# Kernel optimization log

Measured on AMD Instinct MI355X. Metric: run time of the kernel, lower is better.

## Reference

```python
import jax, jax.numpy as jnp
import numpy as np

FEAT_STRIDE = 16
PRE_NMS_TOP_N = 6000
POST_NMS_TOP_N = 300
NMS_THRESH = 0.7
MIN_SIZE = 16.0
SCALES = np.array([8.0, 16.0, 32.0])
RATIOS = np.array([0.5, 1.0, 2.0])


def _whctrs(a):
    w = a[2] - a[0] + 1.0
    h = a[3] - a[1] + 1.0
    return w, h, a[0] + 0.5 * (w - 1.0), a[1] + 0.5 * (h - 1.0)


def _mkanchors(ws, hs, xc, yc):
    ws = np.asarray(ws).reshape(-1, 1)
    hs = np.asarray(hs).reshape(-1, 1)
    return np.hstack([xc - 0.5 * (ws - 1.0), yc - 0.5 * (hs - 1.0),
                      xc + 0.5 * (ws - 1.0), yc + 0.5 * (hs - 1.0)])


def generate_anchors(base_size, ratios, scales):
    base = np.array([1.0, 1.0, base_size, base_size]) - 1.0
    w, h, xc, yc = _whctrs(base)
    size = w * h
    ws = np.round(np.sqrt(size / ratios))
    hs = np.round(ws * ratios)
    ratio_anchors = _mkanchors(ws, hs, xc, yc)
    out = []
    for i in range(ratio_anchors.shape[0]):
        w, h, xc, yc = _whctrs(ratio_anchors[i])
        out.append(_mkanchors(w * scales, h * scales, xc, yc))
    return np.vstack(out)


def _nms(boxes, scores, thresh, max_out):
    # greedy NMS, boxes [N,4], scores [N] (-inf = invalid). Returns idx [max_out], valid [max_out]
    N = boxes.shape[0]
    x1, y1, x2, y2 = boxes[:, 0], boxes[:, 1], boxes[:, 2], boxes[:, 3]
    areas = (x2 - x1 + 1.0) * (y2 - y1 + 1.0)
    ar = jnp.arange(N)

    def step(s, _):
        i = jnp.argmax(s)
        valid = s[i] > -jnp.inf
        b = boxes[i]
        xx1 = jnp.maximum(b[0], x1)
        yy1 = jnp.maximum(b[1], y1)
        xx2 = jnp.minimum(b[2], x2)
        yy2 = jnp.minimum(b[3], y2)
        inter = jnp.maximum(0.0, xx2 - xx1 + 1.0) * jnp.maximum(0.0, yy2 - yy1 + 1.0)
        iou = inter / (areas[i] + areas - inter)
        sup = (iou > thresh) | (ar == i)
        return jnp.where(sup, -jnp.inf, s), (i, valid)

    _, (idx, valid) = jax.lax.scan(step, scores, None, length=max_out)
    return idx, valid


def setup_inputs() -> dict:
    key = jax.random.key(0)
    k1, k2 = jax.random.split(key)
    B, A, Hf, Wf = 16, 9, 160, 160
    scores_map = jax.random.uniform(k1, (B, 2 * A, Hf, Wf), dtype=jnp.float32)
    bbox_deltas = jax.random.normal(k2, (B, 4 * A, Hf, Wf), dtype=jnp.float32) * 0.2
    im_info = jnp.tile(jnp.array([[Hf * FEAT_STRIDE, Wf * FEAT_STRIDE, 1.0]], jnp.float32), (B, 1))
    return {"scores_map": scores_map, "bbox_deltas": bbox_deltas, "im_info": im_info}


def reference(scores_map, bbox_deltas, im_info):
    anchors0 = jnp.asarray(generate_anchors(16, RATIOS, SCALES), jnp.float32)  # [A,4]
    A = anchors0.shape[0]
    B, _, Hf, Wf = scores_map.shape
    # fg scores: [B, A, H, W] -> [B, H*W*A]
    scores = scores_map[:, A:].transpose(0, 2, 3, 1).reshape(B, -1)
    deltas = bbox_deltas.transpose(0, 2, 3, 1).reshape(B, -1, 4)  # [B, H*W*A, 4]
    sx = (jnp.arange(Wf) * FEAT_STRIDE).astype(jnp.float32)
    sy = (jnp.arange(Hf) * FEAT_STRIDE).astype(jnp.float32)
    SX, SY = jnp.meshgrid(sx, sy)  # [H, W]
    shifts = jnp.stack([SX.ravel(), SY.ravel(), SX.ravel(), SY.ravel()], axis=1)  # [K,4]
    all_anchors = (shifts[:, None, :] + anchors0[None, :, :]).reshape(-1, 4)  # [K*A, 4]

    aw = all_anchors[:, 2] - all_anchors[:, 0] + 1.0
    ah = all_anchors[:, 3] - all_anchors[:, 1] + 1.0
    acx = all_anchors[:, 0] + 0.5 * aw
    acy = all_anchors[:, 1] + 0.5 * ah

    def single(s, d, info):
        # bbox_transform_inv
        pcx = d[:, 0] * aw + acx
        pcy = d[:, 1] * ah + acy
        pw = jnp.exp(d[:, 2]) * aw
        ph = jnp.exp(d[:, 3]) * ah
        x1 = jnp.clip(pcx - 0.5 * pw, 0.0, info[1] - 1.0)
        y1 = jnp.clip(pcy - 0.5 * ph, 0.0, info[0] - 1.0)
        x2 = jnp.clip(pcx + 0.5 * pw, 0.0, info[1] - 1.0)
        y2 = jnp.clip(pcy + 0.5 * ph, 0.0, info[0] - 1.0)
        boxes = jnp.stack([x1, y1, x2, y2], axis=1)
        ms = MIN_SIZE * info[2]
        keep = ((x2 - x1 + 1.0) >= ms) & ((y2 - y1 + 1.0) >= ms)
        s = jnp.where(keep, s, -jnp.inf)
        top_s, top_i = jax.lax.top_k(s, PRE_NMS_TOP_N)
        top_b = boxes[top_i]
        idx, valid = _nms(top_b, top_s, NMS_THRESH, POST_NMS_TOP_N)
        return jnp.where(valid[:, None], top_b[idx], 0.0)  # [POST, 4]

    out_boxes = jax.vmap(single)(scores, deltas, im_info)  # [B, POST, 4]
    batch_col = jnp.broadcast_to(
        jnp.arange(B, dtype=out_boxes.dtype)[:, None, None], (B, POST_NMS_TOP_N, 1))
    return jnp.concatenate([batch_col, out_boxes], axis=2)  # [B, POST, 5]
```

## Files before the change

### kernel.cpp

```cpp
#include <hip/hip_runtime.h>
#include <cstdint>
#include <cstddef>

typedef unsigned int u32;
typedef unsigned short u16;
typedef unsigned long long u64;

#define NBATCH 16
#define NA 9
#define HF 160
#define WF 160
#define HWC (HF*WF)
#define NPB (NA*HWC)
#define PRE_N 6000
#define POST_N 300
#define SEL_CAP 8192
#define NBIN 2048
#define UNI_BINS 1024
#define HSLICES 45
#define NMS_W 16
#define CHUNK 512


__constant__ float c_AW[9] = {184.f,368.f,736.f,128.f,256.f,512.f,88.f,176.f,352.f};
__constant__ float c_AH[9] = {96.f,192.f,384.f,128.f,256.f,512.f,176.f,352.f,704.f};

__device__ __forceinline__ void box_core(
    float d0, float d1, float d2, float d3, int a, int x, int y,
    float imH, float imW, float ms,
    float& x1, float& y1, float& x2, float& y2, bool& keep)
{
  float aw = c_AW[a], ah = c_AH[a];
  float acx = (float)x * 16.0f + 8.0f;
  float acy = (float)y * 16.0f + 8.0f;
  float pcx = d0 * aw + acx;
  float pcy = d1 * ah + acy;
  float pw  = expf(d2) * aw;
  float ph  = expf(d3) * ah;
  x1 = fminf(fmaxf(pcx - 0.5f * pw, 0.0f), imW - 1.0f);
  y1 = fminf(fmaxf(pcy - 0.5f * ph, 0.0f), imH - 1.0f);
  x2 = fminf(fmaxf(pcx + 0.5f * pw, 0.0f), imW - 1.0f);
  y2 = fminf(fmaxf(pcy + 0.5f * ph, 0.0f), imH - 1.0f);
  keep = ((x2 - x1 + 1.0f) >= ms) && ((y2 - y1 + 1.0f) >= ms);
}

__device__ __forceinline__ void box_from_deltas(
    const float* __restrict__ bd, int b, int a, int pos,
    float imH, float imW, float ms,
    float& x1, float& y1, float& x2, float& y2, bool& keep)
{
  int y = pos / WF;
  int x = pos - y * WF;
  size_t base = ((size_t)(b * 4 * NA) + 4 * a) * HWC + (size_t)pos;
  float d0 = bd[base];
  float d1 = bd[base + HWC];
  float d2 = bd[base + 2 * HWC];
  float d3 = bd[base + 3 * HWC];
  box_core(d0, d1, d2, d3, a, x, y, imH, imW, ms, x1, y1, x2, y2, keep);
}

__device__ __forceinline__ u32 desc_enc(float s) {
  u32 su = __float_as_uint(s);
  u32 asc = (su & 0x80000000u) ? ~su : (su | 0x80000000u);
  return ~asc;
}

__device__ __forceinline__ bool iou_gt(float inter, float uni) {
  float ss = fmaf(0.7f, uni, -inter);
  if (fabsf(ss) <= uni * 1e-6f) return (inter / uni > 0.7f);
  return ss < 0.0f;
}

__global__ void __launch_bounds__(256) k_scores_hist(
    const float* __restrict__ sm, const float* __restrict__ bd,
    const float* __restrict__ info, u32* __restrict__ keys, u32* __restrict__ hist) {
  __shared__ u32 lh[UNI_BINS];
  int img   = blockIdx.x / HSLICES;
  int rem   = blockIdx.x - img * HSLICES;
  int a     = rem / 5;
  int chunk = rem - a * 5;
  int tid = threadIdx.x;
  for (int i = tid; i < UNI_BINS; i += 256) lh[i] = 0;
  __syncthreads();
  float imH = info[img*3+0], imW = info[img*3+1], ms = 16.0f * info[img*3+2];
  const float* sp = sm + ((size_t)(img * 2 * NA) + NA + a) * HWC;
  const float* dp = bd + ((size_t)(img * 4 * NA) + 4 * a) * HWC;
  u32* kp = keys + (size_t)img * NPB + (size_t)a * HWC;
  for (int j = 0; j < 5; j++) {
    int pos0 = (chunk * 1280 + j * 256 + tid) * 4;
    float4 s4  = *(const float4*)&sp[pos0];
    float4 q0  = *(const float4*)&dp[pos0];
    float4 q1  = *(const float4*)&dp[HWC + pos0];
    float4 q2  = *(const float4*)&dp[2*HWC + pos0];
    float4 q3  = *(const float4*)&dp[3*HWC + pos0];
    float sv[4] = {s4.x, s4.y, s4.z, s4.w};
    float v0[4] = {q0.x, q0.y, q0.z, q0.w};
    float v1[4] = {q1.x, q1.y, q1.z, q1.w};
    float v2[4] = {q2.x, q2.y, q2.z, q2.w};
    float v3[4] = {q3.x, q3.y, q3.z, q3.w};
    u32 kq[4];
    #pragma unroll
    for (int e = 0; e < 4; e++) {
      int pos = pos0 + e;
      int y = pos / WF;
      int x = pos - y * WF;
      float x1, y1, x2, y2; bool keep;
      box_core(v0[e], v1[e], v2[e], v3[e], a, x, y, imH, imW, ms, x1, y1, x2, y2, keep);
      float s = sv[e];
      if (!keep) s = __uint_as_float(0xFF800000u);
      kq[e] = desc_enc(s);
      int q = (int)floorf(s * (float)UNI_BINS);
      q = q < 0 ? 0 : (q > UNI_BINS - 1 ? UNI_BINS - 1 : q);
      atomicAdd(&lh[(UNI_BINS - 1) - q], 1u);
    }
    *(uint4*)&kp[pos0] = make_uint4(kq[0], kq[1], kq[2], kq[3]);
  }
  __syncthreads();
  u32* gh = hist + ((size_t)img * HSLICES + rem) * UNI_BINS;
  ((uint4*)gh)[tid] = make_uint4(lh[4*tid], lh[4*tid+1], lh[4*tid+2], lh[4*tid+3]);
}

__global__ void __launch_bounds__(256) k_select(
    const u32* __restrict__ keys, const u32* __restrict__ hist,
    u64* __restrict__ thresh_arr, u32* __restrict__ selcnt) {
  int img = blockIdx.x, tid = threadIdx.x;
  __shared__ u32 sc[256];
  __shared__ u32 lh[NBIN];
  __shared__ u64 sh_thresh;
  __shared__ int sh_state;
  __shared__ u64 sh_prefix;
  __shared__ u32 sh_kth;
  if (tid == 0) selcnt[img] = 0;
  const u32* gh = hist + (size_t)img * HSLICES * UNI_BINS;
  u32 loc[4] = {0, 0, 0, 0};
  for (int s = 0; s < HSLICES; s++) {
    uint4 v = ((const uint4*)(gh + s * UNI_BINS))[tid];
    loc[0] += v.x; loc[1] += v.y; loc[2] += v.z; loc[3] += v.w;
  }
  u32 tot = loc[0] + loc[1] + loc[2] + loc[3];
  if (tid == 0) { sh_state = 0; sh_prefix = 0; sh_kth = PRE_N; }
  sc[tid] = tot;
  __syncthreads();
  for (int off = 1; off < 256; off <<= 1) {
    u32 v = sc[tid]; u32 a = (tid >= off) ? sc[tid - off] : 0u;
    __syncthreads(); sc[tid] = v + a; __syncthreads();
  }
  u32 incl = sc[tid], excl = incl - tot;
  if (PRE_N > excl && PRE_N <= incl) {
    u32 run = excl;
    #pragma unroll
    for (int j = 0; j < 4; j++) {
      run += loc[j];
      if (run >= PRE_N) {
        int b = tid * 4 + j;
        if (b < UNI_BINS - 1 && run <= SEL_CAP) {
          float sb = (float)(UNI_BINS - 1 - b) * (1.0f / (float)UNI_BINS);
          sh_thresh = ((u64)desc_enc(sb) << 32) | 0xFFFFFFFFull;
          sh_state = 1;
        }
        break;
      }
    }
  }
  __syncthreads();
  if (!sh_state) {
    const u32* kp = keys + (size_t)img * NPB;
    const int shifts[6] = {53, 42, 31, 20, 9, 0};
    const int widths[6] = {11, 11, 11, 11, 11, 9};
    for (int p = 0; p < 6; p++) {
      if (sh_state) break;
      for (int i = tid; i < NBIN; i += 256) lh[i] = 0;
      __syncthreads();
      u64 prefix = sh_prefix; u32 kth = sh_kth;
      int shift = shifts[p], width = widths[p];
      u32 nb = 1u << width;
      int hs = shift + width;
      for (int i = tid; i < NPB; i += 256) {
        int ia = i / HWC;
        int pos = i - ia * HWC;
        u64 key = ((u64)kp[i] << 32) | (u64)(u32)(pos * NA + ia);
        bool m = (p == 0) || ((key >> hs) == prefix);
        if (m) atomicAdd(&lh[(u32)(key >> shift) & (nb - 1u)], 1u);
      }
      __syncthreads();
      u32 l2[8]; u32 t2 = 0;
      #pragma unroll
      for (int j = 0; j < 8; j++) {
        u32 b = (u32)(tid * 8 + j);
        u32 v = (b < nb) ? lh[b] : 0u;
        l2[j] = v; t2 += v;
      }
      sc[tid] = t2; __syncthreads();
      for (int off = 1; off < 256; off <<= 1) {
        u32 v = sc[tid]; u32 a = (tid >= off) ? sc[tid - off] : 0u;
        __syncthreads(); sc[tid] = v + a; __syncthreads();
      }
      u32 incl2 = sc[tid], excl2 = incl2 - t2;
      if (kth > excl2 && kth <= incl2) {
        u32 run = excl2;
        for (int j = 0; j < 8; j++) {
          run += l2[j];
          if (run >= kth) {
            u32 bin = (u32)(tid * 8 + j);
            u32 below = run - l2[j];
            u32 cnt = l2[j];
            u32 knew = kth - below;
            u64 pfull = (prefix << width) | (u64)bin;
            u32 M = (u32)PRE_N - knew + cnt;
            if (M <= SEL_CAP) {
              u64 lowmask = (shift > 0) ? ((1ULL << shift) - 1ULL) : 0ULL;
              sh_thresh = (pfull << shift) | lowmask;
              sh_state = 1;
            } else {
              sh_prefix = pfull; sh_kth = knew;
            }
            break;
          }
        }
      }
      __syncthreads();
    }
  }
  if (tid == 0) thresh_arr[img] = sh_thresh;
}

__global__ void __launch_bounds__(256) k_compact(
    const u32* __restrict__ keys, const u64* __restrict__ thresh,
    u32* __restrict__ selcnt, u64* __restrict__ sel,
    const float* __restrict__ bd, const float* __restrict__ info,
    float4* __restrict__ boxsel) {
  int img = blockIdx.y;
  int tid = threadIdx.x;
  u64 T = thresh[img];
  int t0 = blockIdx.x * 3840;
  const u32* kp = keys + (size_t)img * NPB + t0;
  u64 fk[15];
  u32 mycnt = 0;
  #pragma unroll
  for (int j = 0; j < 15; j++) {
    int t = t0 + j * 256 + tid;
    u32 d = kp[j * 256 + tid];
    int a = t / HWC;
    int pos = t - a * HWC;
    u64 key = ((u64)d << 32) | (u64)(u32)(pos * NA + a);
    fk[j] = key;
    if (key <= T) mycnt++;
  }
  __shared__ u32 sc[256];
  __shared__ u32 sbase;
  sc[tid] = mycnt;
  __syncthreads();
  for (int off = 1; off < 256; off <<= 1) {
    u32 v = sc[tid];
    u32 add = (tid >= off) ? sc[tid - off] : 0u;
    __syncthreads();
    sc[tid] = v + add;
    __syncthreads();
  }
  if (tid == 255 && sc[255] > 0) sbase = atomicAdd(&selcnt[img], sc[255]);
  __syncthreads();
  if (mycnt == 0) return;
  u32 myoff = sbase + sc[tid] - mycnt;
  u64* sp = sel + (size_t)img * SEL_CAP;
  float4* bp = boxsel + (size_t)img * SEL_CAP;
  float imH = info[img*3+0], imW = info[img*3+1], ms = 16.0f * info[img*3+2];
  u32 c = 0;
  #pragma unroll
  for (int j = 0; j < 15; j++) {
    u64 key = fk[j];
    if (key <= T) {
      u32 p = myoff + c;
      if (p < SEL_CAP) {
        u32 desc = (u32)(key >> 32);
        u32 idx = (u32)key;
        sp[p] = ((u64)desc << 31) | ((u64)idx << 13) | (u64)p;
        int a = (int)(idx % NA);
        int pos = (int)(idx / NA);
        float x1, y1, x2, y2; bool keep;
        box_from_deltas(bd, img, a, pos, imH, imW, ms, x1, y1, x2, y2, keep);
        bp[p] = make_float4(x1, y1, x2, y2);
      }
      c++;
    }
  }
}

__global__ void __launch_bounds__(256) k_sort1(u64* __restrict__ sel, const u32* __restrict__ selcnt) {
  __shared__ u64 s[CHUNK];
  int img = blockIdx.y, c = blockIdx.x, tid = threadIdx.x;
  u32 cnt = selcnt[img]; if (cnt > SEL_CAP) cnt = SEL_CAP;
  u64* sp = sel + (size_t)img * SEL_CAP + (size_t)c * CHUNK;
  int gbase = c * CHUNK;
  for (int i = tid; i < CHUNK; i += 256) s[i] = ((u32)(gbase + i) < cnt) ? sp[i] : ~0ULL;
  __syncthreads();
  for (int k = 2; k <= CHUNK; k <<= 1) {
    for (int j = k >> 1; j > 0; j >>= 1) {
      for (int i = tid; i < CHUNK; i += 256) {
        int p = i ^ j;
        if (p > i) {
          u64 a = s[i], b = s[p];
          bool up = ((i & k) == 0);
          if (up ? (a > b) : (a < b)) { s[i] = b; s[p] = a; }
        }
      }
      __syncthreads();
    }
  }
  for (int i = tid; i < CHUNK; i += 256) sp[i] = s[i];
}

__global__ void __launch_bounds__(1024) k_sort2nms(
    const u64* __restrict__ sel, const u32* __restrict__ selcnt,
    const float4* __restrict__ boxsel, float* __restrict__ out) {
  union SB {
    u64 s[SEL_CAP];
    struct {
      u16 slot16[PRE_N + 64];
      float4 kbox[POST_N];
      float karea[POST_N];
      u64 kcodeW[(POST_N + 7) / 8];
      float4 cb[2][64];
      float car[2][64];
      int cint[2][64];
      u64 wcol[2][64];
      u64 supw[2][NMS_W];
    } n;
  };
  __shared__ SB u;
  __shared__ int sh_nv;
  __shared__ int sh_nkept;
  int img = blockIdx.x;
  int tid = threadIdx.x;
  const u64* sp = sel + (size_t)img * SEL_CAP;
  if (tid == 0) { sh_nv = PRE_N; sh_nkept = 0; }
  for (int i = tid; i < SEL_CAP; i += 1024) u.s[i] = sp[i];
  __syncthreads();
  int d0 = tid * 8;
  for (int L = CHUNK; L < SEL_CAP; L <<= 1) {
    bool act = (2 * L < SEL_CAP) || (d0 < PRE_N);
    u64 o[8];
    if (act) {
      int pairBase = d0 & ~(2 * L - 1);
      int d = d0 - pairBase;
      const u64* A = u.s + pairBase;
      const u64* B = u.s + pairBase + L;
      int lo = d - L; if (lo < 0) lo = 0;
      int hi = (d < L) ? d : L;
      while (lo < hi) {
        int mid = (lo + hi) >> 1;
        if (A[mid] <= B[d - 1 - mid]) lo = mid + 1; else hi = mid;
      }
      int ia = lo, ib = d - lo;
      #pragma unroll
      for (int k = 0; k < 8; k++) {
        bool ta = (ib >= L) || (ia < L && A[ia] <= B[ib]);
        o[k] = ta ? A[ia++] : B[ib++];
      }
    }
    __syncthreads();
    if (act) {
      #pragma unroll
      for (int k = 0; k < 8; k++) u.s[d0 + k] = o[k];
    }
    __syncthreads();
  }
  u64 rv[6];
  {
    int k = 0;
    for (int r = tid; r < PRE_N; r += 1024, k++) rv[k] = u.s[r];
    __syncthreads();
    k = 0;
    for (int r = tid; r < PRE_N; r += 1024, k++) {
      u64 key = rv[k];
      u32 desc = (u32)(key >> 31);
      bool valid = desc < 0xFF800000u;
      if (!valid) atomicMin(&sh_nv, r);
      u.n.slot16[r] = valid ? (u16)(key & 0x1FFFu) : (u16)0xFFFF;
    }
  }
  __syncthreads();
  int lane = tid & 63;
  int wv = tid >> 6;
  int nvalid = sh_nv;
  if (nvalid > PRE_N) nvalid = PRE_N;
  const float4* bp = boxsel + (size_t)img * SEL_CAP;
  if (tid < 64) {
    float4 c = make_float4(0.f, 0.f, 0.f, 0.f);
    if (tid < nvalid) { u16 sl = u.n.slot16[tid]; c = bp[sl]; }
    u.n.cb[0][tid] = c;
    float A = (c.z - c.x + 1.0f) * (c.w - c.y + 1.0f);
    u.n.car[0][tid] = A;
    u.n.cint[0][tid] = (int)rintf(8.0f * log2f(A));
  } else if (tid < 128) {
    u.n.wcol[0][tid - 64] = 0;
  } else if (tid < 128 + NMS_W) {
    u.n.supw[0][tid - 128] = 0;
  }
  __syncthreads();
  int pb = 0;
  for (int base = 0; base < nvalid; base += 64, pb ^= 1) {
    int nk = sh_nkept;
    if (nk >= POST_N) break;
    int bn = nvalid - base; if (bn > 64) bn = 64;
    float4 pfc = make_float4(0.f, 0.f, 0.f, 0.f);
    bool havepf = (wv == 1) && (base + 64 < nvalid);
    if (havepf) {
      int i = base + 64 + lane;
      if (i < nvalid) { u16 sl = u.n.slot16[i]; pfc = bp[sl]; }
    }
    bool sup;
    u64 colpart = 0;
    {
      bool inb = lane < bn;
      sup = !inb;
      if (inb) {
        float4 C = u.n.cb[pb][lane];
        float A0 = u.n.car[pb][lane];
        int myc = u.n.cint[pb][lane];
        int nw = (nk + 7) >> 3;
        for (int jw = wv; jw < nw; jw += NMS_W) {
          u64 w = u.n.kcodeW[jw];
          int jbase = jw << 3;
          int jm = nk - jbase; if (jm > 8) jm = 8;
          for (int k = 0; k < jm; k++) {
            int d = (int)((w >> (k * 8)) & 0xFFu) - myc;
            if (d > 5 || d < -5) continue;
            int j = jbase + k;
            float4 K = u.n.kbox[j];
            float xx1 = fmaxf(K.x, C.x);
            float yy1 = fmaxf(K.y, C.y);
            float xx2 = fminf(K.z, C.z);
            float yy2 = fminf(K.w, C.w);
            float iw = fmaxf(0.0f, xx2 - xx1 + 1.0f);
            float ih = fmaxf(0.0f, yy2 - yy1 + 1.0f);
            float inter = iw * ih;
            float uni = (u.n.karea[j] + A0) - inter;
            sup = sup | iou_gt(inter, uni);
          }
        }
        for (int i = wv; i < lane; i += NMS_W) {
          if (i >= bn) break;
          float Ai = u.n.car[pb][i];
          if (Ai <= 0.6999f * A0 || A0 <= 0.6999f * Ai) continue;
          float4 I4 = u.n.cb[pb][i];
          float xx1 = fmaxf(I4.x, C.x);
          float yy1 = fmaxf(I4.y, C.y);
          float xx2 = fminf(I4.z, C.z);
          float yy2 = fminf(I4.w, C.w);
          float iw = fmaxf(0.0f, xx2 - xx1 + 1.0f);
          float ih = fmaxf(0.0f, yy2 - yy1 + 1.0f);
          float inter = iw * ih;
          float uni = (Ai + A0) - inter;
          if (iou_gt(inter, uni)) colpart |= 1ULL << i;
        }
      }
    }
    u64 bm = __ballot(sup);
    if (lane == 0) u.n.supw[pb][wv] = bm;
    if (colpart) atomicOr(&u.n.wcol[pb][lane], colpart);
    if (havepf) {
      u.n.cb[pb ^ 1][lane] = pfc;
      float A = (pfc.z - pfc.x + 1.0f) * (pfc.w - pfc.y + 1.0f);
      u.n.car[pb ^ 1][lane] = A;
      u.n.cint[pb ^ 1][lane] = (int)rintf(8.0f * log2f(A));
    }
    __syncthreads();
    if (wv == 0) {
      u64 so = (lane < NMS_W) ? u.n.supw[pb][lane] : 0ULL;
      so |= __shfl_xor(so, 1);
      so |= __shfl_xor(so, 2);
      so |= __shfl_xor(so, 4);
      so |= __shfl_xor(so, 8);
      so = __shfl(so, 0);
      u64 validm = (bn >= 64) ? ~0ULL : ((1ULL << bn) - 1ULL);
      u64 colm = u.n.wcol[pb][lane];
      u64 live = validm & ~so;
      u64 K = live;
      while (true) {
        u64 supk = __ballot((K & colm) != 0ULL);
        u64 Kn = live & ~supk;
        if (Kn == K) break;
        K = Kn;
      }
      int m = POST_N - nk;
      int kc = (int)__popcll(K);
      if (kc > m) {
        for (int e = kc - m; e > 0; --e) K &= ~(1ULL << (63 - __clzll((long long)K)));
        kc = m;
      }
      int cnt = nk + kc;
      if ((K >> lane) & 1ULL) {
        int rank = nk + (int)__popcll(K & ((1ULL << lane) - 1ULL));
        float4 C = u.n.cb[pb][lane];
        u.n.kbox[rank] = C;
        u.n.karea[rank] = u.n.car[pb][lane];
        ((unsigned char*)u.n.kcodeW)[rank] = (unsigned char)u.n.cint[pb][lane];
        float* o = out + ((size_t)img * POST_N + rank) * 5;
        o[0] = (float)img; o[1] = C.x; o[2] = C.y; o[3] = C.z; o[4] = C.w;
      }
      if (lane == 0) sh_nkept = cnt;
    } else if (wv == 2) {
      u.n.wcol[pb ^ 1][lane] = 0;
      if (lane < NMS_W) u.n.supw[pb ^ 1][lane] = 0;
    }
    __syncthreads();
  }
  int fk = sh_nkept;
  for (int r = fk + tid; r < POST_N; r += NMS_W * 64) {
    float* o = out + ((size_t)img * POST_N + r) * 5;
    o[0] = (float)img; o[1] = 0.f; o[2] = 0.f; o[3] = 0.f; o[4] = 0.f;
  }
}

extern "C" void kernel_launch(void* const* d_in, const int* in_sizes, int n_in,
                              void* d_out, int out_size, void* d_ws, size_t ws_size,
                              hipStream_t stream) {
  const float* sm   = (const float*)d_in[0];
  const float* bd   = (const float*)d_in[1];
  const float* info = (const float*)d_in[2];
  float* out = (float*)d_out;
  char* ws = (char*)d_ws;

  size_t off = 0;
  auto alloc = [&](size_t bytes) { size_t o = off; off += (bytes + 255) & ~(size_t)255; return o; };
  u32* keys     = (u32*)(ws + alloc((size_t)NBATCH * NPB * 4));
  u32* hist     = (u32*)(ws + alloc((size_t)NBATCH * HSLICES * UNI_BINS * 4));
  u32* selcnt   = (u32*)(ws + alloc(NBATCH * 4));
  u64* thresh   = (u64*)(ws + alloc(NBATCH * 8));
  u64* sel      = (u64*)(ws + alloc((size_t)NBATCH * SEL_CAP * 8));
  float4* boxsel= (float4*)(ws + alloc((size_t)NBATCH * SEL_CAP * 16));
  (void)ws_size; (void)in_sizes; (void)n_in; (void)out_size;

  hipLaunchKernelGGL(k_scores_hist, dim3(NBATCH * HSLICES), dim3(256), 0, stream, sm, bd, info, keys, hist);
  hipLaunchKernelGGL(k_select, dim3(16), dim3(256), 0, stream, keys, hist, thresh, selcnt);
  hipLaunchKernelGGL(k_compact, dim3(60, 16), dim3(256), 0, stream, keys, thresh, selcnt, sel, bd, info, boxsel);
  hipLaunchKernelGGL(k_sort1, dim3(SEL_CAP / CHUNK, 16), dim3(256), 0, stream, sel, selcnt);
  hipLaunchKernelGGL(k_sort2nms, dim3(16), dim3(1024), 0, stream, sel, selcnt, boxsel, out);
}
```

Baseline: 190.4 us.

## Process NMS candidates in 128-wide blocks as two 64-lane halves per iteration

The block-parallel greedy NMS now handles 128 candidates per outer iteration instead of 64. Each lane tests two candidates against the kept boxes, computes intra-half suppression masks plus a cross mask from the first half to the second, and wave 0 resolves the halves one after the other. The aim is to halve the number of barrier-separated iterations and amortise the scan over kept boxes. The cost is more per-lane work, more shared memory, and wasted work when the 300-box cap is reached in the first half.

```diff
diff --git a/kernel.cpp b/kernel.cpp
--- a/kernel.cpp
+++ b/kernel.cpp
@@ -69,6 +69,19 @@
   float ss = fmaf(0.7f, uni, -inter);
   if (fabsf(ss) <= uni * 1e-6f) return (inter / uni > 0.7f);
   return ss < 0.0f;
+}
+
+__device__ __forceinline__ bool sup_test(const float4& E, float Ae,
+                                         const float4& C, float Ac) {
+  float xx1 = fmaxf(E.x, C.x);
+  float yy1 = fmaxf(E.y, C.y);
+  float xx2 = fminf(E.z, C.z);
+  float yy2 = fminf(E.w, C.w);
+  float iw = fmaxf(0.0f, xx2 - xx1 + 1.0f);
+  float ih = fmaxf(0.0f, yy2 - yy1 + 1.0f);
+  float inter = iw * ih;
+  float uni = (Ae + Ac) - inter;
+  return iou_gt(inter, uni);
 }
 
 __global__ void __launch_bounds__(256) k_scores_hist(
@@ -319,11 +332,13 @@
       float4 kbox[POST_N];
       float karea[POST_N];
       u64 kcodeW[(POST_N + 7) / 8];
-      float4 cb[2][64];
-      float car[2][64];
-      int cint[2][64];
-      u64 wcol[2][64];
-      u64 supw[2][NMS_W];
+      float4 cb[2][128];
+      float car[2][128];
+      int cint[2][128];
+      u64 wcol[2][128];
+      u64 xcol[2][64];
+      u64 supw1[2][NMS_W];
+      u64 supw2[2][NMS_W];
     } n;
   };
   __shared__ SB u;
@@ -384,101 +399,119 @@
   int nvalid = sh_nv;
   if (nvalid > PRE_N) nvalid = PRE_N;
   const float4* bp = boxsel + (size_t)img * SEL_CAP;
-  if (tid < 64) {
+  if (tid < 128) {
     float4 c = make_float4(0.f, 0.f, 0.f, 0.f);
     if (tid < nvalid) { u16 sl = u.n.slot16[tid]; c = bp[sl]; }
     u.n.cb[0][tid] = c;
     float A = (c.z - c.x + 1.0f) * (c.w - c.y + 1.0f);
     u.n.car[0][tid] = A;
     u.n.cint[0][tid] = (int)rintf(8.0f * log2f(A));
-  } else if (tid < 128) {
-    u.n.wcol[0][tid - 64] = 0;
-  } else if (tid < 128 + NMS_W) {
-    u.n.supw[0][tid - 128] = 0;
+  } else if (tid < 256) {
+    u.n.wcol[0][tid - 128] = 0;
+  } else if (tid < 320) {
+    u.n.xcol[0][tid - 256] = 0;
+  } else if (tid < 320 + NMS_W) {
+    u.n.supw1[0][tid - 320] = 0;
+  } else if (tid < 336 + NMS_W) {
+    u.n.supw2[0][tid - 336] = 0;
   }
   __syncthreads();
   int pb = 0;
-  for (int base = 0; base < nvalid; base += 64, pb ^= 1) {
+  for (int base = 0; base < nvalid; base += 128, pb ^= 1) {
     int nk = sh_nkept;
     if (nk >= POST_N) break;
-    int bn = nvalid - base; if (bn > 64) bn = 64;
+    int bn = nvalid - base; if (bn > 128) bn = 128;
+    int bn1 = bn > 64 ? 64 : bn;
+    int bn2 = bn - bn1;
     float4 pfc = make_float4(0.f, 0.f, 0.f, 0.f);
-    bool havepf = (wv == 1) && (base + 64 < nvalid);
+    bool havepf = ((wv == 1) && (base + 128 < nvalid)) ||
+                  ((wv == 3) && (base + 192 < nvalid));
+    int pfslot = (wv == 1) ? lane : 64 + lane;
     if (havepf) {
-      int i = base + 64 + lane;
+      int i = base + 128 + pfslot;
       if (i < nvalid) { u16 sl = u.n.slot16[i]; pfc = bp[sl]; }
     }
-    bool sup;
-    u64 colpart = 0;
+    bool sup1, sup2;
+    u64 col1 = 0, col2 = 0, x2m = 0;
     {
-      bool inb = lane < bn;
-      sup = !inb;
-      if (inb) {
-        float4 C = u.n.cb[pb][lane];
-        float A0 = u.n.car[pb][lane];
-        int myc = u.n.cint[pb][lane];
+      bool inb1 = lane < bn1;
+      bool inb2 = lane < bn2;
+      sup1 = !inb1; sup2 = !inb2;
+      float4 C1, C2; float A01 = 0.f, A02 = 0.f; int myc1 = 0, myc2 = 0;
+      if (inb1) { C1 = u.n.cb[pb][lane];      A01 = u.n.car[pb][lane];      myc1 = u.n.cint[pb][lane]; }
+      if (inb2) { C2 = u.n.cb[pb][64 + lane]; A02 = u.n.car[pb][64 + lane]; myc2 = u.n.cint[pb][64 + lane]; }
+      if (inb1 || inb2) {
         int nw = (nk + 7) >> 3;
         for (int jw = wv; jw < nw; jw += NMS_W) {
           u64 w = u.n.kcodeW[jw];
           int jbase = jw << 3;
           int jm = nk - jbase; if (jm > 8) jm = 8;
           for (int k = 0; k < jm; k++) {
-            int d = (int)((w >> (k * 8)) & 0xFFu) - myc;
-            if (d > 5 || d < -5) continue;
+            int code = (int)((w >> (k * 8)) & 0xFFu);
+            int d1 = code - myc1, d2 = code - myc2;
+            bool g1 = inb1 && d1 <= 5 && d1 >= -5;
+            bool g2 = inb2 && d2 <= 5 && d2 >= -5;
+            if (!g1 && !g2) continue;
             int j = jbase + k;
             float4 K = u.n.kbox[j];
-            float xx1 = fmaxf(K.x, C.x);
-            float yy1 = fmaxf(K.y, C.y);
-            float xx2 = fminf(K.z, C.z);
-            float yy2 = fminf(K.w, C.w);
-            float iw = fmaxf(0.0f, xx2 - xx1 + 1.0f);
-            float ih = fmaxf(0.0f, yy2 - yy1 + 1.0f);
-            float inter = iw * ih;
-            float uni = (u.n.karea[j] + A0) - inter;
-            sup = sup | iou_gt(inter, uni);
+            float Ka = u.n.karea[j];
+            if (g1) sup1 = sup1 | sup_test(K, Ka, C1, A01);
+            if (g2) sup2 = sup2 | sup_test(K, Ka, C2, A02);
           }
         }
-        for (int i = wv; i < lane; i += NMS_W) {
-          if (i >= bn) break;
-          float Ai = u.n.car[pb][i];
-          if (Ai <= 0.6999f * A0 || A0 <= 0.6999f * Ai) continue;
-          float4 I4 = u.n.cb[pb][i];
-          float xx1 = fmaxf(I4.x, C.x);
-          float yy1 = fmaxf(I4.y, C.y);
-          float xx2 = fminf(I4.z, C.z);
-          float yy2 = fminf(I4.w, C.w);
-          float iw = fmaxf(0.0f, xx2 - xx1 + 1.0f);
-          float ih = fmaxf(0.0f, yy2 - yy1 + 1.0f);
-          float inter = iw * ih;
-          float uni = (Ai + A0) - inter;
-          if (iou_gt(inter, uni)) colpart |= 1ULL << i;
-        }
-      }
-    }
-    u64 bm = __ballot(sup);
-    if (lane == 0) u.n.supw[pb][wv] = bm;
-    if (colpart) atomicOr(&u.n.wcol[pb][lane], colpart);
+        if (inb1) {
+          for (int i = wv; i < lane; i += NMS_W) {
+            if (i >= bn1) break;
+            float Ai = u.n.car[pb][i];
+            if (Ai <= 0.6999f * A01 || A01 <= 0.6999f * Ai) continue;
+            if (sup_test(u.n.cb[pb][i], Ai, C1, A01)) col1 |= 1ULL << i;
+          }
+        }
+        if (inb2) {
+          for (int i = wv; i < lane; i += NMS_W) {
+            if (i >= bn2) break;
+            float Ai = u.n.car[pb][64 + i];
+            if (Ai <= 0.6999f * A02 || A02 <= 0.6999f * Ai) continue;
+            if (sup_test(u.n.cb[pb][64 + i], Ai, C2, A02)) col2 |= 1ULL << i;
+          }
+          for (int i = wv; i < bn1; i += NMS_W) {
+            float Ai = u.n.car[pb][i];
+            if (Ai <= 0.6999f * A02 || A02 <= 0.6999f * Ai) continue;
+            if (sup_test(u.n.cb[pb][i], Ai, C2, A02)) x2m |= 1ULL << i;
+          }
+        }
+      }
+    }
+    u64 bm1 = __ballot(sup1);
+    u64 bm2 = __ballot(sup2);
+    if (lane == 0) { u.n.supw1[pb][wv] = bm1; u.n.supw2[pb][wv] = bm2; }
+    if (col1) atomicOr(&u.n.wcol[pb][lane], col1);
+    if (col2) atomicOr(&u.n.wcol[pb][64 + lane], col2);
+    if (x2m)  atomicOr(&u.n.xcol[pb][lane], x2m);
     if (havepf) {
-      u.n.cb[pb ^ 1][lane] = pfc;
+      u.n.cb[pb ^ 1][pfslot] = pfc;
       float A = (pfc.z - pfc.x + 1.0f) * (pfc.w - pfc.y + 1.0f);
-      u.n.car[pb ^ 1][lane] = A;
-      u.n.cint[pb ^ 1][lane] = (int)rintf(8.0f * log2f(A));
+      u.n.car[pb ^ 1][pfslot] = A;
+      u.n.cint[pb ^ 1][pfslot] = (int)rintf(8.0f * log2f(A));
     }
     __syncthreads();
     if (wv == 0) {
-      u64 so = (lane < NMS_W) ? u.n.supw[pb][lane] : 0ULL;
-      so |= __shfl_xor(so, 1);
-      so |= __shfl_xor(so, 2);
-      so |= __shfl_xor(so, 4);
-      so |= __shfl_xor(so, 8);
-      so = __shfl(so, 0);
-      u64 validm = (bn >= 64) ? ~0ULL : ((1ULL << bn) - 1ULL);
-      u64 colm = u.n.wcol[pb][lane];
-      u64 live = validm & ~so;
-      u64 K = live;
+      u64 so1 = (lane < NMS_W) ? u.n.supw1[pb][lane] : 0ULL;
+      so1 |= __shfl_xor(so1, 1); so1 |= __shfl_xor(so1, 2);
+      so1 |= __shfl_xor(so1, 4); so1 |= __shfl_xor(so1, 8);
+      so1 = __shfl(so1, 0);
+      u64 so2 = (lane < NMS_W) ? u.n.supw2[pb][lane] : 0ULL;
+      so2 |= __shfl_xor(so2, 1); so2 |= __shfl_xor(so2, 2);
+      so2 |= __shfl_xor(so2, 4); so2 |= __shfl_xor(so2, 8);
+      so2 = __shfl(so2, 0);
+      u64 valid1 = (bn1 >= 64) ? ~0ULL : ((1ULL << bn1) - 1ULL);
+      u64 valid2 = (bn2 >= 64) ? ~0ULL : (bn2 ? ((1ULL << bn2) - 1ULL) : 0ULL);
+      u64 colm1 = u.n.wcol[pb][lane];
+      u64 live1 = valid1 & ~so1;
+      u64 K = live1;
       while (true) {
-        u64 supk = __ballot((K & colm) != 0ULL);
-        u64 Kn = live & ~supk;
+        u64 sk = __ballot((K & colm1) != 0ULL);
+        u64 Kn = live1 & ~sk;
         if (Kn == K) break;
         K = Kn;
       }
@@ -488,7 +521,7 @@
         for (int e = kc - m; e > 0; --e) K &= ~(1ULL << (63 - __clzll((long long)K)));
         kc = m;
       }
-      int cnt = nk + kc;
+      int nk1 = nk + kc;
       if ((K >> lane) & 1ULL) {
         int rank = nk + (int)__popcll(K & ((1ULL << lane) - 1ULL));
         float4 C = u.n.cb[pb][lane];
@@ -498,10 +531,41 @@
         float* o = out + ((size_t)img * POST_N + rank) * 5;
         o[0] = (float)img; o[1] = C.x; o[2] = C.y; o[3] = C.z; o[4] = C.w;
       }
-      if (lane == 0) sh_nkept = cnt;
+      if (nk1 < POST_N && bn2 > 0) {
+        u64 xm = u.n.xcol[pb][lane];
+        u64 sup2x = __ballot((xm & K) != 0ULL);
+        u64 colm2 = u.n.wcol[pb][64 + lane];
+        u64 live2 = valid2 & ~so2 & ~sup2x;
+        u64 K2 = live2;
+        while (true) {
+          u64 sk = __ballot((K2 & colm2) != 0ULL);
+          u64 Kn = live2 & ~sk;
+          if (Kn == K2) break;
+          K2 = Kn;
+        }
+        int m2 = POST_N - nk1;
+        int kc2 = (int)__popcll(K2);
+        if (kc2 > m2) {
+          for (int e = kc2 - m2; e > 0; --e) K2 &= ~(1ULL << (63 - __clzll((long long)K2)));
+          kc2 = m2;
+        }
+        if ((K2 >> lane) & 1ULL) {
+          int rank = nk1 + (int)__popcll(K2 & ((1ULL << lane) - 1ULL));
+          float4 C = u.n.cb[pb][64 + lane];
+          u.n.kbox[rank] = C;
+          u.n.karea[rank] = u.n.car[pb][64 + lane];
+          ((unsigned char*)u.n.kcodeW)[rank] = (unsigned char)u.n.cint[pb][64 + lane];
+          float* o = out + ((size_t)img * POST_N + rank) * 5;
+          o[0] = (float)img; o[1] = C.x; o[2] = C.y; o[3] = C.z; o[4] = C.w;
+        }
+        nk1 += kc2;
+      }
+      if (lane == 0) sh_nkept = nk1;
     } else if (wv == 2) {
       u.n.wcol[pb ^ 1][lane] = 0;
-      if (lane < NMS_W) u.n.supw[pb ^ 1][lane] = 0;
+      u.n.wcol[pb ^ 1][64 + lane] = 0;
+      u.n.xcol[pb ^ 1][lane] = 0;
+      if (lane < NMS_W) { u.n.supw1[pb ^ 1][lane] = 0; u.n.supw2[pb ^ 1][lane] = 0; }
     }
     __syncthreads();
   }
```

Result: slower. 197.1 us (+3.5%).
